# Kernel optimization log

Hardware: AMD Instinct MI355X
Metric: run time of the kernel (lower is better)

The kernel has to match this reference:

```python
import jax, jax.numpy as jnp
import numpy as np

N_HEADS = 8  # init n_heads

def setup_inputs() -> dict:
    key = jax.random.key(0)
    ks = jax.random.split(key, 5)
    hid = 128  # = init hidden_dim // 2
    h = jax.random.normal(ks[0], (4, 4097, hid), dtype=jnp.float32)  # n=4096 nodes + 1 aux node
    init = lambda k, shp, fan: jax.random.normal(k, shp, dtype=jnp.float32) / np.float32(np.sqrt(fan))
    W_q = init(ks[1], (hid, hid), hid)        # stored (in, out); torch Linear applies x @ W.T
    W_kv = init(ks[2], (hid, 2 * hid), hid)
    W_mhc = init(ks[3], (hid, hid), hid)
    W_lin = init(ks[4], (2, 1), 2)            # (2, edge_out_dim)
    return {"h": h, "W_q": W_q, "W_kv": W_kv, "W_mhc": W_mhc, "W_lin": W_lin}

def reference(h, W_q, W_kv, W_mhc, W_lin):
    # aux_node=True: last row is the graph embedding h_g
    hn, hg = h[:, :-1, :], h[:, -1:, :]
    bp, n, hid = hn.shape
    D = hid // N_HEADS  # head_dim
    # single-query multi-head attention: q from aux node, k/v from nodes
    q = (hg @ W_q).reshape(bp, 1, N_HEADS, D).transpose(0, 2, 1, 3)       # (bp,H,1,D)
    kv = hn @ W_kv
    k = kv[..., :hid].reshape(bp, n, N_HEADS, D).transpose(0, 2, 1, 3)    # (bp,H,n,D)
    v = kv[..., hid:].reshape(bp, n, N_HEADS, D).transpose(0, 2, 1, 3)    # (bp,H,n,D)
    scale = 1.0 / jnp.sqrt(jnp.float32(D))
    attn = jax.nn.softmax(jnp.einsum('bhqd,bhkd->bhqk', q, k) * scale, axis=-1)
    y = jnp.einsum('bhqk,bhkd->bhqd', attn, v)                            # (bp,H,1,D)
    y = y.transpose(0, 2, 1, 3).reshape(bp, 1, hid)
    mh = y @ W_mhc                                                        # (bp,1,hid)
    # per-node scalar score: y2[b,i] = <mh[b], hn[b,i]>
    y2 = jnp.einsum('boh,bnh->bn', mh, hn)                                # (bp,n)
    # pairwise edge features [y_j, y_i] -> linear(2->edge_out_dim), fused as
    # e[b,i,j,o] = y2[b,j]*W_lin[0,o] + y2[b,i]*W_lin[1,o]
    e = y2[:, None, :, None] * W_lin[0] + y2[:, :, None, None] * W_lin[1]  # (bp,n,n,E)
    return e.reshape(bp, n * n, W_lin.shape[1])
```

## Files before the change

### kernel.cpp

```cpp
#include <hip/hip_runtime.h>
#include <hip/hip_bf16.h>
#include <math.h>

#define HID 128
#define NH  8
#define DH  16
#define NN  4096
#define BP  4
#define SEQ 4097

#define WS_S   0
#define WS_T   131072
#define WS_L   (WS_T + 4096)
#define WS_A   (WS_L + 32)
#define WS_B   (WS_A + 16384)

__global__ void kA_score(const float* __restrict__ h,
                         const float* __restrict__ W_q,
                         const float* __restrict__ W_kv,
                         float* __restrict__ ws) {
    __shared__ float hg_sh[HID];
    __shared__ float q_sh[HID];
    __shared__ float u_sh[NH * HID];
    __shared__ float red[256];
    const int blk = blockIdx.x;
    const int b = blk >> 7;
    const int jb = (blk & 127) * 32;
    const int t = threadIdx.x;
    const float* hb = h + (size_t)b * SEQ * HID;

    if (t < HID) hg_sh[t] = hb[(size_t)NN * HID + t];
    __syncthreads();
    if (t < HID) {
        float a = 0.f;
        #pragma unroll 8
        for (int c = 0; c < HID; ++c) a = fmaf(hg_sh[c], W_q[c * HID + t], a);
        q_sh[t] = a;
    }
    __syncthreads();
    for (int i = t; i < NH * HID; i += 256) {
        const int hh = i >> 7, c = i & 127;
        float a = 0.f;
        #pragma unroll
        for (int d = 0; d < DH; ++d)
            a = fmaf(W_kv[c * 2 * HID + hh * DH + d], q_sh[hh * DH + d], a);
        u_sh[i] = a * 0.25f;
    }
    __syncthreads();

    const int hh = t & 7;
    const int j = jb + (t >> 3);
    const float4* hrow = (const float4*)(hb + (size_t)j * HID);
    const float4* uu = (const float4*)(u_sh + hh * HID);
    float acc = 0.f;
    #pragma unroll
    for (int c4 = 0; c4 < HID / 4; ++c4) {
        float4 hv = hrow[c4];
        float4 uv = uu[c4];
        acc = fmaf(hv.x, uv.x, acc);
        acc = fmaf(hv.y, uv.y, acc);
        acc = fmaf(hv.z, uv.z, acc);
        acc = fmaf(hv.w, uv.w, acc);
    }
    ws[WS_S + ((size_t)b * NH + hh) * NN + j] = acc;

    red[t] = __expf(acc);
    __syncthreads();
    #pragma unroll
    for (int off = 128; off >= 8; off >>= 1) {
        if (t < off) red[t] += red[t + off];
        __syncthreads();
    }
    if (t < 8) atomicAdd(ws + WS_L + b * NH + t, red[t]);
}

__global__ void kC_weighted(const float* __restrict__ h,
                            float* __restrict__ ws) {
    __shared__ float p_sh[NH * 32];
    __shared__ float rl_sh[NH];
    const int blk = blockIdx.x;
    const int b = blk >> 7;
    const int j0 = (blk & 127) * 32;
    const int t = threadIdx.x;

    if (t < NH) rl_sh[t] = 1.0f / ws[WS_L + b * NH + t];
    __syncthreads();
    {
        const int hh = t >> 5, j = t & 31;
        p_sh[t] = __expf(ws[WS_S + ((size_t)b * NH + hh) * NN + j0 + j]) * rl_sh[hh];
    }
    __syncthreads();

    const int c = t & 127;
    const int jh = t >> 7;
    float acc[NH];
    #pragma unroll
    for (int hh = 0; hh < NH; ++hh) acc[hh] = 0.f;

    const float* hb = h + (size_t)b * SEQ * HID;
    for (int j = jh; j < 32; j += 2) {
        float hv = hb[(size_t)(j0 + j) * HID + c];
        #pragma unroll
        for (int hh = 0; hh < NH; ++hh)
            acc[hh] = fmaf(p_sh[hh * 32 + j], hv, acc[hh]);
    }
    float* tb = ws + WS_T + (size_t)b * NH * HID;
    #pragma unroll
    for (int hh = 0; hh < NH; ++hh)
        atomicAdd(tb + hh * HID + c, acc[hh]);
}

__global__ void kE_y2(const float* __restrict__ h,
                      const float* __restrict__ W_kv,
                      const float* __restrict__ W_mhc,
                      const float* __restrict__ W_lin,
                      float* __restrict__ ws) {
    __shared__ float y_sh[HID];
    __shared__ float mh_sh[HID];
    const int blk = blockIdx.x;
    const int b = blk >> 5;
    const int t = threadIdx.x;
    const int j = (blk & 31) * 128 + t;

    const float* tb = ws + WS_T + (size_t)b * NH * HID;
    const int hh = t >> 4;
    float a = 0.f;
    #pragma unroll 8
    for (int c = 0; c < HID; ++c)
        a = fmaf(tb[hh * HID + c], W_kv[c * 2 * HID + HID + t], a);
    y_sh[t] = a;
    __syncthreads();
    float mo = 0.f;
    #pragma unroll 8
    for (int hd = 0; hd < HID; ++hd)
        mo = fmaf(y_sh[hd], W_mhc[hd * HID + t], mo);
    mh_sh[t] = mo;
    __syncthreads();

    const float4* hrow = (const float4*)(h + (size_t)b * SEQ * HID + (size_t)j * HID);
    const float4* mm = (const float4*)mh_sh;
    float acc = 0.f;
    #pragma unroll
    for (int c4 = 0; c4 < HID / 4; ++c4) {
        float4 hv = hrow[c4];
        float4 mv = mm[c4];
        acc = fmaf(hv.x, mv.x, acc);
        acc = fmaf(hv.y, mv.y, acc);
        acc = fmaf(hv.z, mv.z, acc);
        acc = fmaf(hv.w, mv.w, acc);
    }
    ws[WS_A + (size_t)b * NN + j] = W_lin[0] * acc;
    ws[WS_B + (size_t)b * NN + j] = W_lin[1] * acc;
}

__global__ void kF_emit(const float* __restrict__ ws,
                        float* __restrict__ out) {
    const int blk = blockIdx.x;
    const int b = blk >> 12;
    const int i = blk & (NN - 1);
    const float add = ws[WS_B + (size_t)b * NN + i];
    const float4* arow = (const float4*)(ws + WS_A + (size_t)b * NN);
    float4* orow = (float4*)(out + ((size_t)b << 24) + ((size_t)i << 12));
    #pragma unroll
    for (int k = threadIdx.x; k < NN / 4; k += 256) {
        float4 v = arow[k];
        v.x += add; v.y += add; v.z += add; v.w += add;
        orow[k] = v;
    }
}

extern "C" void kernel_launch(void* const* d_in, const int* in_sizes, int n_in,
                              void* d_out, int out_size, void* d_ws, size_t ws_size,
                              hipStream_t stream) {
    const float* h     = (const float*)d_in[0];
    const float* W_q   = (const float*)d_in[1];
    const float* W_kv  = (const float*)d_in[2];
    const float* W_mhc = (const float*)d_in[3];
    const float* W_lin = (const float*)d_in[4];
    float* out = (float*)d_out;
    float* ws = (float*)d_ws;

    hipMemsetAsync(ws + WS_T, 0, (4096 + 32) * sizeof(float), stream);

    kA_score<<<BP * 128, 256, 0, stream>>>(h, W_q, W_kv, ws);
    kC_weighted<<<BP * 128, 256, 0, stream>>>(h, ws);
    kE_y2<<<BP * 32, 128, 0, stream>>>(h, W_kv, W_mhc, W_lin, ws);
    kF_emit<<<BP * NN, 256, 0, stream>>>(ws, out);
}
```

Measured before the change: 329.6 us.

## Fuse score and weighted-sum kernels, defer softmax normalization, use nontemporal output stores

The score kernel now keeps the unnormalized exp weights in shared memory and accumulates the weighted sum of node rows directly, so the separate weighted-sum kernel and its round-trip of scores through global memory go away. Division by the softmax denominator moves into the y2 kernel, after the value projection. The u_sh buffer is padded to reduce LDS bank conflicts, and the large output write uses nontemporal vector stores. The cost is dominated by the 268 MB output write, so the savings from fusion are small relative to the total, and nontemporal stores may change write throughput either way.

```diff
diff --git a/kernel.cpp b/kernel.cpp
--- a/kernel.cpp
+++ b/kernel.cpp
@@ -1,5 +1,4 @@
 #include <hip/hip_runtime.h>
-#include <hip/hip_bf16.h>
 #include <math.h>
 
 #define HID 128
@@ -9,23 +8,27 @@
 #define BP  4
 #define SEQ 4097
 
-#define WS_S   0
-#define WS_T   131072
-#define WS_L   (WS_T + 4096)
-#define WS_A   (WS_L + 32)
-#define WS_B   (WS_A + 16384)
+#define WS_T   0
+#define WS_L   4096
+#define WS_A   4128
+#define WS_B   (WS_A + BP * NN)
 
-__global__ void kA_score(const float* __restrict__ h,
-                         const float* __restrict__ W_q,
-                         const float* __restrict__ W_kv,
-                         float* __restrict__ ws) {
+#define UPAD 132
+
+typedef float f32x4 __attribute__((ext_vector_type(4)));
+
+__global__ void k1_score_acc(const float* __restrict__ h,
+                             const float* __restrict__ W_q,
+                             const float* __restrict__ W_kv,
+                             float* __restrict__ ws) {
     __shared__ float hg_sh[HID];
     __shared__ float q_sh[HID];
-    __shared__ float u_sh[NH * HID];
+    __shared__ float u_sh[NH * UPAD];
+    __shared__ float p_sh[256];
     __shared__ float red[256];
     const int blk = blockIdx.x;
     const int b = blk >> 7;
-    const int jb = (blk & 127) * 32;
+    const int j0 = (blk & 127) * 32;
     const int t = threadIdx.x;
     const float* hb = h + (size_t)b * SEQ * HID;
 
@@ -44,14 +47,14 @@
         #pragma unroll
         for (int d = 0; d < DH; ++d)
             a = fmaf(W_kv[c * 2 * HID + hh * DH + d], q_sh[hh * DH + d], a);
-        u_sh[i] = a * 0.25f;
+        u_sh[hh * UPAD + c] = a * 0.25f;
     }
     __syncthreads();
 
     const int hh = t & 7;
-    const int j = jb + (t >> 3);
-    const float4* hrow = (const float4*)(hb + (size_t)j * HID);
-    const float4* uu = (const float4*)(u_sh + hh * HID);
+    const int jl = t >> 3;
+    const float4* hrow = (const float4*)(hb + (size_t)(j0 + jl) * HID);
+    const float4* uu = (const float4*)(u_sh + hh * UPAD);
     float acc = 0.f;
     #pragma unroll
     for (int c4 = 0; c4 < HID / 4; ++c4) {
@@ -62,9 +65,9 @@
         acc = fmaf(hv.z, uv.z, acc);
         acc = fmaf(hv.w, uv.w, acc);
     }
-    ws[WS_S + ((size_t)b * NH + hh) * NN + j] = acc;
-
-    red[t] = __expf(acc);
+    const float p = __expf(acc);
+    p_sh[t] = p;
+    red[t] = p;
     __syncthreads();
     #pragma unroll
     for (int off = 128; off >= 8; off >>= 1) {
@@ -72,42 +75,22 @@
         __syncthreads();
     }
     if (t < 8) atomicAdd(ws + WS_L + b * NH + t, red[t]);
-}
-
-__global__ void kC_weighted(const float* __restrict__ h,
-                            float* __restrict__ ws) {
-    __shared__ float p_sh[NH * 32];
-    __shared__ float rl_sh[NH];
-    const int blk = blockIdx.x;
-    const int b = blk >> 7;
-    const int j0 = (blk & 127) * 32;
-    const int t = threadIdx.x;
-
-    if (t < NH) rl_sh[t] = 1.0f / ws[WS_L + b * NH + t];
-    __syncthreads();
-    {
-        const int hh = t >> 5, j = t & 31;
-        p_sh[t] = __expf(ws[WS_S + ((size_t)b * NH + hh) * NN + j0 + j]) * rl_sh[hh];
-    }
-    __syncthreads();
 
     const int c = t & 127;
     const int jh = t >> 7;
-    float acc[NH];
+    float acc2[NH];
     #pragma unroll
-    for (int hh = 0; hh < NH; ++hh) acc[hh] = 0.f;
-
-    const float* hb = h + (size_t)b * SEQ * HID;
+    for (int k = 0; k < NH; ++k) acc2[k] = 0.f;
     for (int j = jh; j < 32; j += 2) {
         float hv = hb[(size_t)(j0 + j) * HID + c];
         #pragma unroll
-        for (int hh = 0; hh < NH; ++hh)
-            acc[hh] = fmaf(p_sh[hh * 32 + j], hv, acc[hh]);
+        for (int k = 0; k < NH; ++k)
+            acc2[k] = fmaf(p_sh[j * 8 + k], hv, acc2[k]);
     }
     float* tb = ws + WS_T + (size_t)b * NH * HID;
     #pragma unroll
-    for (int hh = 0; hh < NH; ++hh)
-        atomicAdd(tb + hh * HID + c, acc[hh]);
+    for (int k = 0; k < NH; ++k)
+        atomicAdd(tb + k * HID + c, acc2[k]);
 }
 
 __global__ void kE_y2(const float* __restrict__ h,
@@ -128,7 +111,7 @@
     #pragma unroll 8
     for (int c = 0; c < HID; ++c)
         a = fmaf(tb[hh * HID + c], W_kv[c * 2 * HID + HID + t], a);
-    y_sh[t] = a;
+    y_sh[t] = a / ws[WS_L + b * NH + hh];
     __syncthreads();
     float mo = 0.f;
     #pragma unroll 8
@@ -159,13 +142,12 @@
     const int b = blk >> 12;
     const int i = blk & (NN - 1);
     const float add = ws[WS_B + (size_t)b * NN + i];
-    const float4* arow = (const float4*)(ws + WS_A + (size_t)b * NN);
-    float4* orow = (float4*)(out + ((size_t)b << 24) + ((size_t)i << 12));
+    const f32x4* arow = (const f32x4*)(ws + WS_A + (size_t)b * NN);
+    f32x4* orow = (f32x4*)(out + ((size_t)b << 24) + ((size_t)i << 12));
     #pragma unroll
     for (int k = threadIdx.x; k < NN / 4; k += 256) {
-        float4 v = arow[k];
-        v.x += add; v.y += add; v.z += add; v.w += add;
-        orow[k] = v;
+        f32x4 v = arow[k] + add;
+        __builtin_nontemporal_store(v, orow + k);
     }
 }
 
@@ -182,8 +164,7 @@
 
     hipMemsetAsync(ws + WS_T, 0, (4096 + 32) * sizeof(float), stream);
 
-    kA_score<<<BP * 128, 256, 0, stream>>>(h, W_q, W_kv, ws);
-    kC_weighted<<<BP * 128, 256, 0, stream>>>(h, ws);
+    k1_score_acc<<<BP * 128, 256, 0, stream>>>(h, W_q, W_kv, ws);
     kE_y2<<<BP * 32, 128, 0, stream>>>(h, W_kv, W_mhc, W_lin, ws);
     kF_emit<<<BP * NN, 256, 0, stream>>>(ws, out);
 }
```

After: 322.6 us. -2.1%, faster.
